# Performance work log

Measured on AMD Instinct MI355X. Metric: run time of the kernel, lower is better.

## Reference

```python
import jax, jax.numpy as jnp
import numpy as np
from jax.scipy.stats import norm

B, IN, H0, H1, OUT = 1024, 2048, 4096, 4096, 1000
EPS_CDF = 1e-5
DECAY = 0.01
NEG_SLOPE = 0.01  # LeakyReLU default slope


def setup_inputs() -> dict:
    key = jax.random.key(0)
    ks = iter(jax.random.split(key, 40))
    rn = lambda shp, s=1.0: s * jax.random.normal(next(ks), shp, dtype=jnp.float32)
    inp = {}
    inp['x'] = rn((B, IN))
    inp['z_w'] = rn((IN,), 0.02)
    for nm, (o, i) in zip(['0', '1', 'o'], [(H0, IN), (H1, H0), (OUT, H1)]):
        inp['w_mu' + nm] = rn((o, i), 0.02)
        inp['w_ls' + nm] = rn((o, i), 0.1) - 2.0  # log-sigma ~ -2 => sigma ~ 0.13
        inp['b_mu' + nm] = rn((o,), 0.02)
        inp['b_ls' + nm] = rn((o,), 0.1) - 2.0
        inp['eps_w' + nm] = rn((o, i))
        inp['eps_b' + nm] = rn((o,))
    inp['pfz0'] = jax.random.uniform(next(ks), (B, H0), dtype=jnp.float32)
    inp['pfz1'] = jax.random.uniform(next(ks), (B, H1), dtype=jnp.float32)
    inp['y'] = jax.random.randint(next(ks), (B,), 0, OUT, dtype=jnp.int32)
    inp['mz0'] = jax.random.randint(next(ks), (B, H0), 0, 2, dtype=jnp.int32)
    inp['mz1'] = jax.random.randint(next(ks), (B, H1), 0, 2, dtype=jnp.int32)
    inp['mask_mu0'] = jax.random.randint(next(ks), (H0,), 0, 2, dtype=jnp.int32)
    inp['mask_mu1'] = jax.random.randint(next(ks), (H1,), 0, 2, dtype=jnp.int32)
    inp['data_set_size'] = 60000
    return inp


def _bayes_layer(h, w_mu, w_ls, b_mu, b_ls, eps_w, eps_b, mz, mask_mu, pfz):
    sw = jnp.exp(w_ls)
    sb = jnp.exp(b_ls)
    w = w_mu + sw * eps_w          # reparameterized weight sample
    b = b_mu + sb * eps_b
    h = h @ w.T + b                # F.linear
    h = jnp.where(h >= 0, h, NEG_SLOPE * h)  # LeakyReLU
    mzf = mz.astype(h.dtype)
    m = mzf * mask_mu.astype(h.dtype)[None, :]   # [B, h]
    mult = m.shape[1] / (m.sum(1) + 1e-6)        # rescale multiplier per sample
    h = h * m * mult[:, None]
    # GFN forward-flow log-prob of the z-mask
    p = jnp.clip(pfz, 1e-6, 1.0 - 1e-6)
    flow = (mzf * jnp.log(p) + (1.0 - mzf) * jnp.log(1.0 - p)).sum()
    # Gaussian CDF likelihood of sampled weights/biases (finite-difference density)
    pw = norm.cdf(w + EPS_CDF, w_mu, sw) - norm.cdf(w - EPS_CDF, w_mu, sw)
    pb = norm.cdf(b + EPS_CDF, b_mu, sb) - norm.cdf(b - EPS_CDF, b_mu, sb)
    flow = flow + jnp.log(pw).sum() + jnp.log(pb).sum()
    return h, flow


def reference(x, z_w, w_mu0, w_ls0, b_mu0, b_ls0, eps_w0, eps_b0,
              w_mu1, w_ls1, b_mu1, b_ls1, eps_w1, eps_b1,
              w_muo, w_lso, b_muo, b_lso, eps_wo, eps_bo,
              pfz0, pfz1, y, mz0, mz1, mask_mu0, mask_mu1, data_set_size):
    loss = (x @ z_w).sum()  # total flow estimator Z
    h, f0 = _bayes_layer(x, w_mu0, w_ls0, b_mu0, b_ls0, eps_w0, eps_b0, mz0, mask_mu0, pfz0)
    loss = loss + f0
    h, f1 = _bayes_layer(h, w_mu1, w_ls1, b_mu1, b_ls1, eps_w1, eps_b1, mz1, mask_mu1, pfz1)
    loss = loss + f1
    # output BayesLinear (sampled)
    wo = w_muo + jnp.exp(w_lso) * eps_wo
    bo = b_muo + jnp.exp(b_lso) * eps_bo
    pred = h @ wo.T + bo  # [B, OUT]
    logp = jax.nn.log_softmax(pred, axis=-1)
    ce = -jnp.take_along_axis(logp, y[:, None].astype(jnp.int32), axis=1).mean()
    loss = loss + jnp.float32(data_set_size) * ce  # NLL
    wd = DECAY * ((w_mu0 ** 2).sum() + jnp.exp(w_ls0).sum()
                  + (w_mu1 ** 2).sum() + jnp.exp(w_ls1).sum())
    loss = (loss + wd) ** 2
    return pred, loss
```

## Files before the change

kernel.cpp:

```cpp
#include <hip/hip_runtime.h>
#include <math.h>

#define B_SZ 1024
#define IN_SZ 2048
#define H0_SZ 4096
#define H1_SZ 4096
#define OUT_SZ 1000

typedef _Float16 f16;
typedef __attribute__((ext_vector_type(4))) _Float16 f16x4;
typedef __attribute__((ext_vector_type(8))) _Float16 f16x8;
typedef __attribute__((ext_vector_type(4))) float f32x4;

#define OFF_N0     0ULL
#define OFF_N1     4ULL
#define OFF_MSUM0  256ULL
#define OFF_MSUM1  4352ULL
#define OFF_CPOS0  8448ULL
#define OFF_CPOS1  24832ULL
#define OFF_IDX0   41216ULL
#define OFF_IDX1   57600ULL
#define OFF_PXZ    73984ULL
#define OFF_PFL    82176ULL
#define OFF_PCE    98560ULL
#define OFF_PB     106752ULL
#define OFF_PW     107776ULL
#define OFF_BS0    370688ULL
#define OFF_BS1    387072ULL
#define OFF_BSO    403456ULL
#define OFF_XH     407552ULL
#define OFF_XL     4601856ULL
#define OFF_H0H    8796160ULL
#define OFF_H0L    17184768ULL
#define OFF_H1H    25573376ULL
#define OFF_H1L    33961984ULL
#define OFF_W0CH   42350592ULL
#define OFF_W0CL   59127808ULL
#define OFF_W1CH   75905024ULL
#define OFF_W1CL   109459456ULL
#define OFF_WOCH   143013888ULL
#define OFF_WOCL   151402496ULL
#define OFF_PART   159791104ULL

#define PSTRIDE_H  2560
#define PSTRIDE_O  1024

__device__ __forceinline__ void gload_lds16(const void* g, void* l)
{
    __builtin_amdgcn_global_load_lds((const __attribute__((address_space(1))) void*)g,
                                     (__attribute__((address_space(3))) void*)l, 16, 0, 0);
}

__device__ __forceinline__ void reduce4_store(double v0, double v1, double v2, double v3,
                                              double* dst)
{
    __shared__ double sh[4][4];
    double v[4] = {v0, v1, v2, v3};
    int lane = threadIdx.x & 63, wid = threadIdx.x >> 6;
#pragma unroll
    for (int a = 0; a < 4; ++a) {
        double x = v[a];
#pragma unroll
        for (int o = 32; o > 0; o >>= 1) x += __shfl_down(x, o, 64);
        if (lane == 0) sh[a][wid] = x;
    }
    __syncthreads();
    if (threadIdx.x == 0) {
        dst[0] = sh[0][0] + sh[0][1] + sh[0][2] + sh[0][3];
        dst[1] = sh[1][0] + sh[1][1] + sh[1][2] + sh[1][3];
        dst[2] = sh[2][0] + sh[2][1] + sh[2][2] + sh[2][3];
        dst[3] = sh[3][0] + sh[3][1] + sh[3][2] + sh[3][3];
    }
}

__device__ __forceinline__ void reduce1_store(double v, double* dst)
{
    __shared__ double sh1[4];
    int lane = threadIdx.x & 63, wid = threadIdx.x >> 6;
#pragma unroll
    for (int o = 32; o > 0; o >>= 1) v += __shfl_down(v, o, 64);
    if (lane == 0) sh1[wid] = v;
    __syncthreads();
    if (threadIdx.x == 0) dst[0] = sh1[0] + sh1[1] + sh1[2] + sh1[3];
}

__global__ __launch_bounds__(1024) void idxbuild_kernel(
    const int* __restrict__ mask0, const int* __restrict__ mask1,
    int* __restrict__ cpos0, int* __restrict__ idx0, int* __restrict__ n0,
    int* __restrict__ cpos1, int* __restrict__ idx1, int* __restrict__ n1)
{
    __shared__ int sh[1024];
    const int t = threadIdx.x;
    for (int pass = 0; pass < 2; ++pass) {
        const int* mask = pass ? mask1 : mask0;
        int* cpos = pass ? cpos1 : cpos0;
        int* idx = pass ? idx1 : idx0;
        int* np = pass ? n1 : n0;
        int4 m = ((const int4*)mask)[t];
        int s = m.x + m.y + m.z + m.w;
        sh[t] = s;
        __syncthreads();
        for (int o = 1; o < 1024; o <<= 1) {
            int v = (t >= o) ? sh[t - o] : 0;
            __syncthreads();
            sh[t] += v;
            __syncthreads();
        }
        int run = sh[t] - s;
        int4 cp;
        cp.x = run; cp.y = run + m.x; cp.z = cp.y + m.y; cp.w = cp.z + m.z;
        ((int4*)cpos)[t] = cp;
        if (m.x) idx[cp.x] = 4 * t + 0;
        if (m.y) idx[cp.y] = 4 * t + 1;
        if (m.z) idx[cp.z] = 4 * t + 2;
        if (m.w) idx[cp.w] = 4 * t + 3;
        if (t == 1023) *np = sh[1023];
        __syncthreads();
    }
}

__global__ __launch_bounds__(256) void splitx_kernel(const float4* __restrict__ x,
                                                     const float4* __restrict__ zw,
                                                     f16x4* __restrict__ xh, f16x4* __restrict__ xl,
                                                     double* __restrict__ pxz)
{
    const int n4 = B_SZ * IN_SZ / 4;
    double s = 0;
    int i = blockIdx.x * blockDim.x + threadIdx.x;
    int stride = gridDim.x * blockDim.x;
    for (; i < n4; i += stride) {
        float4 v = x[i];
        float4 z = zw[i & (IN_SZ / 4 - 1)];
        s += (double)v.x * z.x + (double)v.y * z.y + (double)v.z * z.z + (double)v.w * z.w;
        f16 h0 = (f16)v.x, h1 = (f16)v.y, h2 = (f16)v.z, h3 = (f16)v.w;
        f16x4 hv = {h0, h1, h2, h3};
        f16x4 lv = {(f16)(v.x - (float)h0), (f16)(v.y - (float)h1),
                    (f16)(v.z - (float)h2), (f16)(v.w - (float)h3)};
        xh[i] = hv; xl[i] = lv;
    }
    reduce1_store(s, pxz + blockIdx.x);
}

__global__ __launch_bounds__(256) void flowmsum_kernel(const int* __restrict__ mz,
                                                       const float* __restrict__ pfz,
                                                       const int* __restrict__ maskmu,
                                                       float* __restrict__ msum,
                                                       double* __restrict__ pfl)
{
    const int b = blockIdx.x;
    const int4* m4 = (const int4*)(mz + (size_t)b * 4096);
    const float4* p4 = (const float4*)(pfz + (size_t)b * 4096);
    const int4* k4 = (const int4*)maskmu;
    int s = 0;
    double fl = 0;
    for (int i = threadIdx.x; i < 1024; i += 256) {
        int4 m = m4[i];
        float4 p = p4[i];
        int4 k = k4[i];
        s += m.x * k.x + m.y * k.y + m.z * k.z + m.w * k.w;
        float a0 = fminf(fmaxf(p.x, 1e-6f), 1.0f - 1e-6f);
        float a1 = fminf(fmaxf(p.y, 1e-6f), 1.0f - 1e-6f);
        float a2 = fminf(fmaxf(p.z, 1e-6f), 1.0f - 1e-6f);
        float a3 = fminf(fmaxf(p.w, 1e-6f), 1.0f - 1e-6f);
        fl += (double)logf(m.x ? a0 : 1.0f - a0);
        fl += (double)logf(m.y ? a1 : 1.0f - a1);
        fl += (double)logf(m.z ? a2 : 1.0f - a2);
        fl += (double)logf(m.w ? a3 : 1.0f - a3);
    }
#pragma unroll
    for (int o = 32; o > 0; o >>= 1) {
        s += __shfl_down(s, o, 64);
        fl += __shfl_down(fl, o, 64);
    }
    __shared__ int shi[4];
    __shared__ double shd[4];
    if ((threadIdx.x & 63) == 0) { shi[threadIdx.x >> 6] = s; shd[threadIdx.x >> 6] = fl; }
    __syncthreads();
    if (threadIdx.x == 0) {
        msum[b] = (float)(shi[0] + shi[1] + shi[2] + shi[3]);
        pfl[b] = shd[0] + shd[1] + shd[2] + shd[3];
    }
}

template <int RED>
__global__ __launch_bounds__(256) void bsample_kernel(const float* __restrict__ bmu,
                                                      const float* __restrict__ bls,
                                                      const float* __restrict__ beps,
                                                      float* __restrict__ out, int n,
                                                      double* __restrict__ pb)
{
    int i = blockIdx.x * 256 + threadIdx.x;
    float l = 0.f, e = 0.f;
    if (i < n) {
        l = bls[i]; e = beps[i];
        out[i] = fmaf(__expf(l), e, bmu[i]);
    }
    if (RED) {
        double sls = (i < n) ? (double)l : 0.0;
        double se2 = (i < n) ? (double)e * e : 0.0;
        reduce4_store(sls, se2, 0.0, 0.0, pb + (size_t)blockIdx.x * 4);
    }
}

__global__ __launch_bounds__(256) void wsample_rowc_kernel(
    const float* __restrict__ mu, const float* __restrict__ ls, const float* __restrict__ eps,
    const int* __restrict__ maskR, const int* __restrict__ cposR,
    f16* __restrict__ hi, double* __restrict__ pw)
{
    const int r = blockIdx.x;
    const size_t rb = (size_t)r * IN_SZ;
    const float4* m4 = (const float4*)(mu + rb);
    const float4* l4 = (const float4*)(ls + rb);
    const float4* e4 = (const float4*)(eps + rb);
    const bool wr_ = maskR[r] != 0;
    const int drow = cposR[r];
    f16* hrow = hi + (size_t)drow * IN_SZ;
    double sls = 0, se2 = 0, smu2 = 0, sex = 0;
    for (int i = threadIdx.x; i < IN_SZ / 4; i += 256) {
        float4 m = m4[i], l = l4[i], e = e4[i];
        float g0 = __expf(l.x), g1 = __expf(l.y), g2 = __expf(l.z), g3 = __expf(l.w);
        float w0 = fmaf(g0, e.x, m.x), w1 = fmaf(g1, e.y, m.y);
        float w2 = fmaf(g2, e.z, m.z), w3 = fmaf(g3, e.w, m.w);
        sls += (double)l.x + l.y + l.z + l.w;
        se2 += (double)e.x * e.x + (double)e.y * e.y + (double)e.z * e.z + (double)e.w * e.w;
        smu2 += (double)m.x * m.x + (double)m.y * m.y + (double)m.z * m.z + (double)m.w * m.w;
        sex += (double)g0 + g1 + g2 + g3;
        if (wr_) {
            f16x4 hv = {(f16)w0, (f16)w1, (f16)w2, (f16)w3};
            *(f16x4*)(hrow + i * 4) = hv;
        }
    }
    reduce4_store(sls, se2, smu2, sex, pw + (size_t)r * 4);
}

template <int ROWC, int RED>
__global__ __launch_bounds__(256) void wsample_colc_kernel(
    const float* __restrict__ mu, const float* __restrict__ ls, const float* __restrict__ eps,
    const int* __restrict__ maskR, const int* __restrict__ cposR,
    const int* __restrict__ maskC, const int* __restrict__ cposC, const int* __restrict__ pNc,
    f16* __restrict__ hi, double* __restrict__ pw)
{
    __shared__ __align__(16) f16 ldsH[4096];
    const int r = blockIdx.x;
    const size_t rb = (size_t)r * 4096;
    const float4* m4 = (const float4*)(mu + rb);
    const float4* l4 = (const float4*)(ls + rb);
    const float4* e4 = (const float4*)(eps + rb);
    const bool wr_ = ROWC ? (maskR[r] != 0) : true;
    const int drow = ROWC ? cposR[r] : r;
    const int t = threadIdx.x;
    const f16x8 z8 = {0, 0, 0, 0, 0, 0, 0, 0};
    for (int i = t; i < 512; i += 256) ((f16x8*)ldsH)[i] = z8;
    __syncthreads();
    double sls = 0, se2 = 0, smu2 = 0, sex = 0;
    for (int i = t; i < 1024; i += 256) {
        float4 m = m4[i], l = l4[i], e = e4[i];
        float g0 = __expf(l.x), g1 = __expf(l.y), g2 = __expf(l.z), g3 = __expf(l.w);
        float w0 = fmaf(g0, e.x, m.x), w1 = fmaf(g1, e.y, m.y);
        float w2 = fmaf(g2, e.z, m.z), w3 = fmaf(g3, e.w, m.w);
        if (RED) {
            sls += (double)l.x + l.y + l.z + l.w;
            se2 += (double)e.x * e.x + (double)e.y * e.y + (double)e.z * e.z + (double)e.w * e.w;
            smu2 += (double)m.x * m.x + (double)m.y * m.y + (double)m.z * m.z + (double)m.w * m.w;
            sex += (double)g0 + g1 + g2 + g3;
        }
        if (wr_) {
            int4 mc = ((const int4*)maskC)[i];
            int4 cp = ((const int4*)cposC)[i];
            if (mc.x) ldsH[cp.x] = (f16)w0;
            if (mc.y) ldsH[cp.y] = (f16)w1;
            if (mc.z) ldsH[cp.z] = (f16)w2;
            if (mc.w) ldsH[cp.w] = (f16)w3;
        }
    }
    __syncthreads();
    if (wr_) {
        const int n8 = ((*pNc + 127) >> 7) << 4;
        f16x8* hd = (f16x8*)(hi + (size_t)drow * 4096);
        for (int i = t; i < n8; i += 256) hd[i] = ((const f16x8*)ldsH)[i];
    }
    if (RED) reduce4_store(sls, se2, smu2, sex, pw + (size_t)r * 4);
}

template <int NSPLIT>
__global__ __launch_bounds__(256, 3) void mg128b(
    const f16* __restrict__ Ah, const f16* __restrict__ Al, int SA,
    const f16* __restrict__ Wh, int SW,
    const int* __restrict__ pN, int NFIX,
    const int* __restrict__ pK, int KFIX,
    float* __restrict__ P0, float* __restrict__ P1,
    float* __restrict__ P2, float* __restrict__ P3,
    float* __restrict__ P4, float* __restrict__ P5,
    float* __restrict__ P6, float* __restrict__ P7, int pstride)
{
    const int bid = blockIdx.x;
    const int c8 = bid & 7, j = bid >> 3;
    int nt, mt, z;
    if (NSPLIT == 4) {
        const int p = c8 + 8 * (j % 10);
        nt = p >> 2; z = p & 3; mt = j / 10;
    } else {
        const int p = c8 + 8 * (j & 7);
        nt = p >> 3; z = p & 7; mt = j >> 3;
    }
    const int nvalid = pN ? *pN : NFIX;
    const int bn = nt * 128;
    if (bn >= nvalid) return;
    const int bm = mt * 128;
    const int kvalid = pK ? *pK : KFIX;
    const int ktiles = (kvalid + 31) >> 5;
    const int prt = (ktiles + NSPLIT - 1) / NSPLIT;
    const int kt0 = z * prt;
    const int kt1 = min(ktiles, kt0 + prt);
    float* Cf = (z == 0) ? P0 : (z == 1) ? P1 : (z == 2) ? P2 : (z == 3) ? P3
              : (z == 4) ? P4 : (z == 5) ? P5 : (z == 6) ? P6 : P7;

    __shared__ __align__(16) f16 lds[2][12288];
    const int tid = threadIdx.x;
    const int wv = tid >> 6, lane = tid & 63;
    const int wr = wv >> 1, wc = wv & 1;
    const int l15 = lane & 15, l4 = lane >> 4;

    const f16* sg[6];
    int ldst[6];
#pragma unroll
    for (int i = 0; i < 6; ++i) {
        const int c = wv * 6 + i;
        const int plane = c >> 3, cidx = c & 7;
        const f16* base = (plane == 0) ? Ah : (plane == 1) ? Al : Wh;
        const int S_ = (plane < 2) ? SA : SW;
        const int rowb = (plane < 2) ? bm : bn;
        sg[i] = base + (size_t)(rowb + cidx * 16 + l15) * S_ + l4 * 8;
        ldst[i] = c * 512 + lane * 8;
    }

#define STAGE(KT, B) do { \
        _Pragma("unroll") \
        for (int i_ = 0; i_ < 6; ++i_) \
            gload_lds16(sg[i_] + (size_t)(KT) * 32, &lds[B][ldst[i_]]); \
    } while (0)

    f32x4 acc[4][4];
#pragma unroll
    for (int m = 0; m < 4; ++m)
#pragma unroll
        for (int n = 0; n < 4; ++n) acc[m][n] = (f32x4){0.f, 0.f, 0.f, 0.f};

    if (kt0 < kt1) {
        STAGE(kt0, 0);
        int cur = 0;
        for (int kt = kt0; kt < kt1; ++kt) {
            asm volatile("s_waitcnt vmcnt(0)" ::: "memory");
            __builtin_amdgcn_s_barrier();
            __builtin_amdgcn_sched_barrier(0);
            if (kt + 1 < kt1) STAGE(kt + 1, cur ^ 1);
            __builtin_amdgcn_sched_barrier(0);
            const f16* L = &lds[cur][0];
            f16x8 ah[4], al[4], wh[4];
#pragma unroll
            for (int m = 0; m < 4; ++m) {
                ah[m] = *(const f16x8*)(L + (wr * 4 + m) * 512 + lane * 8);
                al[m] = *(const f16x8*)(L + 4096 + (wr * 4 + m) * 512 + lane * 8);
            }
#pragma unroll
            for (int n = 0; n < 4; ++n)
                wh[n] = *(const f16x8*)(L + 8192 + (wc * 4 + n) * 512 + lane * 8);
#pragma unroll
            for (int m = 0; m < 4; ++m)
#pragma unroll
                for (int n = 0; n < 4; ++n)
                    acc[m][n] = __builtin_amdgcn_mfma_f32_16x16x32_f16(ah[m], wh[n], acc[m][n], 0, 0, 0);
#pragma unroll
            for (int m = 0; m < 4; ++m)
#pragma unroll
                for (int n = 0; n < 4; ++n)
                    acc[m][n] = __builtin_amdgcn_mfma_f32_16x16x32_f16(al[m], wh[n], acc[m][n], 0, 0, 0);
            cur ^= 1;
        }
    }
#undef STAGE

#pragma unroll
    for (int n = 0; n < 4; ++n) {
        const int c = bn + wc * 64 + n * 16 + l15;
        if (c >= pstride) continue;
#pragma unroll
        for (int m = 0; m < 4; ++m)
#pragma unroll
            for (int j2 = 0; j2 < 4; ++j2) {
                const int row = bm + wr * 64 + m * 16 + l4 * 4 + j2;
                Cf[(size_t)row * pstride + c] = acc[m][n][j2];
            }
    }
}

__global__ __launch_bounds__(256) void combine4_kernel(
    const float* __restrict__ PA, const float* __restrict__ PB,
    const float* __restrict__ PC, const float* __restrict__ PD, int pstride,
    const float* __restrict__ bsamp, const int* __restrict__ idx,
    const int* __restrict__ mz, const float* __restrict__ msum,
    const int* __restrict__ pN,
    f16* __restrict__ Chh, f16* __restrict__ Chl)
{
    const int nv = *pN;
    const int bn = blockIdx.x * 64;
    const int bm = blockIdx.y * 64;
    const int t = threadIdx.x;
    const int c0 = bn + (t & 15) * 4;
    const int r0 = bm + (t >> 4);
#pragma unroll
    for (int rr = 0; rr < 4; ++rr) {
        const int row = r0 + rr * 16;
        const float mult = 4096.0f / (msum[row] + 1e-6f);
        float sv[4] = {0.f, 0.f, 0.f, 0.f};
        if (c0 < pstride) {
            float4 a = *(const float4*)(PA + (size_t)row * pstride + c0);
            float4 b = *(const float4*)(PB + (size_t)row * pstride + c0);
            float4 c = *(const float4*)(PC + (size_t)row * pstride + c0);
            float4 d = *(const float4*)(PD + (size_t)row * pstride + c0);
            sv[0] = (a.x + b.x) + (c.x + d.x);
            sv[1] = (a.y + b.y) + (c.y + d.y);
            sv[2] = (a.z + b.z) + (c.z + d.z);
            sv[3] = (a.w + b.w) + (c.w + d.w);
        }
        f16 hh[4], ll[4];
#pragma unroll
        for (int jj = 0; jj < 4; ++jj) {
            const int c = c0 + jj;
            float v = 0.f;
            if (c < nv) {
                const int orig = idx[c];
                v = sv[jj] + bsamp[orig];
                v = v >= 0.f ? v : 0.01f * v;
                v = v * (float)mz[(size_t)row * 4096 + orig] * mult;
            }
            hh[jj] = (f16)v;
            ll[jj] = (f16)(v - (float)hh[jj]);
        }
        f16x4 hv = {hh[0], hh[1], hh[2], hh[3]};
        f16x4 lv = {ll[0], ll[1], ll[2], ll[3]};
        *(f16x4*)(Chh + (size_t)row * 4096 + c0) = hv;
        *(f16x4*)(Chl + (size_t)row * 4096 + c0) = lv;
    }
}

__global__ __launch_bounds__(256) void ce_fused8_kernel(
    const float* __restrict__ Q0, const float* __restrict__ Q1,
    const float* __restrict__ Q2, const float* __restrict__ Q3,
    const float* __restrict__ Q4, const float* __restrict__ Q5,
    const float* __restrict__ Q6, const float* __restrict__ Q7,
    const float* __restrict__ bso, const int* __restrict__ y,
    float* __restrict__ pred, double* __restrict__ pce)
{
    const int b = blockIdx.x;
    float mx = -1e30f;
    for (int jj = threadIdx.x; jj < OUT_SZ; jj += 256) {
        const size_t o = (size_t)b * PSTRIDE_O + jj;
        float v = ((Q0[o] + Q1[o]) + (Q2[o] + Q3[o]))
                + ((Q4[o] + Q5[o]) + (Q6[o] + Q7[o])) + bso[jj];
        pred[(size_t)b * OUT_SZ + jj] = v;
        mx = fmaxf(mx, v);
    }
#pragma unroll
    for (int o = 32; o > 0; o >>= 1) mx = fmaxf(mx, __shfl_down(mx, o, 64));
    __shared__ float sm[4];
    if ((threadIdx.x & 63) == 0) sm[threadIdx.x >> 6] = mx;
    __syncthreads();
    mx = fmaxf(fmaxf(sm[0], sm[1]), fmaxf(sm[2], sm[3]));
    double se = 0;
    for (int jj = threadIdx.x; jj < OUT_SZ; jj += 256)
        se += (double)__expf(pred[(size_t)b * OUT_SZ + jj] - mx);
#pragma unroll
    for (int o = 32; o > 0; o >>= 1) se += __shfl_down(se, o, 64);
    __shared__ double sd[4];
    if ((threadIdx.x & 63) == 0) sd[threadIdx.x >> 6] = se;
    __syncthreads();
    if (threadIdx.x == 0) {
        double lse = (double)mx + log(sd[0] + sd[1] + sd[2] + sd[3]);
        pce[b] = lse - (double)pred[(size_t)b * OUT_SZ + y[b]];
    }
}

__global__ __launch_bounds__(256) void finalize_kernel(
    const double* __restrict__ PXZ, const double* __restrict__ PFL,
    const double* __restrict__ PCE, const double* __restrict__ PB,
    const double* __restrict__ PW, const int* __restrict__ dss, float* __restrict__ out)
{
    const int t = threadIdx.x;
    double xz = 0, fl = 0, ce = 0, ls = 0, e2 = 0, mu2 = 0, ex = 0;
    for (int i = t; i < 1024; i += 256) xz += PXZ[i];
    for (int i = t; i < 2048; i += 256) fl += PFL[i];
    for (int i = t; i < 1024; i += 256) ce += PCE[i];
    for (int i = t; i < 8192; i += 256) {
        const double* p = PW + (size_t)i * 4;
        ls += p[0]; e2 += p[1]; mu2 += p[2]; ex += p[3];
    }
    if (t < 32) { ls += PB[t * 4]; e2 += PB[t * 4 + 1]; }
    __shared__ double sh[7][4];
    double v[7] = {xz, fl, ce, ls, e2, mu2, ex};
    const int lane = t & 63, wid = t >> 6;
#pragma unroll
    for (int a = 0; a < 7; ++a) {
        double x = v[a];
#pragma unroll
        for (int o = 32; o > 0; o >>= 1) x += __shfl_down(x, o, 64);
        if (lane == 0) sh[a][wid] = x;
    }
    __syncthreads();
    if (t == 0) {
        double T[7];
#pragma unroll
        for (int a = 0; a < 7; ++a) T[a] = sh[a][0] + sh[a][1] + sh[a][2] + sh[a][3];
        const double NTOT = 25174016.0;
        double cst = NTOT * (log(2.0e-5) - 0.91893853320467274178);
        double loss = T[0]
                    + cst - T[3] - 0.5 * T[4]
                    + T[1]
                    + (double)(*dss) * (T[2] / (double)B_SZ)
                    + 0.01 * (T[5] + T[6]);
        out[(size_t)B_SZ * OUT_SZ] = (float)(loss * loss);
    }
}

extern "C" void kernel_launch(void* const* d_in, const int* in_sizes, int n_in,
                              void* d_out, int out_size, void* d_ws, size_t ws_size,
                              hipStream_t stream)
{
    const float* x = (const float*)d_in[0];
    const float* zw = (const float*)d_in[1];
    const float* wmu0 = (const float*)d_in[2];
    const float* wls0 = (const float*)d_in[3];
    const float* bmu0 = (const float*)d_in[4];
    const float* bls0 = (const float*)d_in[5];
    const float* weps0 = (const float*)d_in[6];
    const float* beps0 = (const float*)d_in[7];
    const float* wmu1 = (const float*)d_in[8];
    const float* wls1 = (const float*)d_in[9];
    const float* bmu1 = (const float*)d_in[10];
    const float* bls1 = (const float*)d_in[11];
    const float* weps1 = (const float*)d_in[12];
    const float* beps1 = (const float*)d_in[13];
    const float* wmuo = (const float*)d_in[14];
    const float* wlso = (const float*)d_in[15];
    const float* bmuo = (const float*)d_in[16];
    const float* blso = (const float*)d_in[17];
    const float* wepso = (const float*)d_in[18];
    const float* bepso = (const float*)d_in[19];
    const float* pfz0 = (const float*)d_in[20];
    const float* pfz1 = (const float*)d_in[21];
    const int* y = (const int*)d_in[22];
    const int* mz0 = (const int*)d_in[23];
    const int* mz1 = (const int*)d_in[24];
    const int* mmu0 = (const int*)d_in[25];
    const int* mmu1 = (const int*)d_in[26];
    const int* dss = (const int*)d_in[27];

    char* ws = (char*)d_ws;
    int* n0p = (int*)(ws + OFF_N0);
    int* n1p = (int*)(ws + OFF_N1);
    float* msum0 = (float*)(ws + OFF_MSUM0);
    float* msum1 = (float*)(ws + OFF_MSUM1);
    int* cpos0 = (int*)(ws + OFF_CPOS0);
    int* cpos1 = (int*)(ws + OFF_CPOS1);
    int* idx0 = (int*)(ws + OFF_IDX0);
    int* idx1 = (int*)(ws + OFF_IDX1);
    double* PXZ = (double*)(ws + OFF_PXZ);
    double* PFL = (double*)(ws + OFF_PFL);
    double* PCE = (double*)(ws + OFF_PCE);
    double* PB = (double*)(ws + OFF_PB);
    double* PW = (double*)(ws + OFF_PW);
    float* bs0 = (float*)(ws + OFF_BS0);
    float* bs1 = (float*)(ws + OFF_BS1);
    float* bso = (float*)(ws + OFF_BSO);
    f16* xh = (f16*)(ws + OFF_XH);
    f16* xl = (f16*)(ws + OFF_XL);
    f16* h0h = (f16*)(ws + OFF_H0H);
    f16* h0l = (f16*)(ws + OFF_H0L);
    f16* h1h = (f16*)(ws + OFF_H1H);
    f16* h1l = (f16*)(ws + OFF_H1L);
    f16* w0ch = (f16*)(ws + OFF_W0CH);
    f16* w1ch = (f16*)(ws + OFF_W1CH);
    f16* woch = (f16*)(ws + OFF_WOCH);
    float* out = (float*)d_out;

    float* A0 = (float*)(ws + OFF_H1H);
    float* A1 = (float*)(ws + OFF_PART);
    float* A2 = (float*)(ws + OFF_W0CL);
    float* A3 = (float*)(ws + OFF_W1CL);
    float* B0 = (float*)(ws + OFF_W0CH);
    float* B1 = (float*)(ws + OFF_W0CL);
    float* B2 = (float*)(ws + OFF_W1CL);
    float* B3 = (float*)(ws + OFF_PART);
    float* Q[8];
    for (int i = 0; i < 8; ++i) Q[i] = (float*)(ws + OFF_W0CH + (size_t)i * 4194304ULL);

    splitx_kernel<<<1024, 256, 0, stream>>>((const float4*)x, (const float4*)zw,
                                            (f16x4*)xh, (f16x4*)xl, PXZ);
    flowmsum_kernel<<<B_SZ, 256, 0, stream>>>(mz0, pfz0, mmu0, msum0, PFL);
    flowmsum_kernel<<<B_SZ, 256, 0, stream>>>(mz1, pfz1, mmu1, msum1, PFL + 1024);
    bsample_kernel<1><<<16, 256, 0, stream>>>(bmu0, bls0, beps0, bs0, H0_SZ, PB);
    bsample_kernel<1><<<16, 256, 0, stream>>>(bmu1, bls1, beps1, bs1, H1_SZ, PB + 16 * 4);
    bsample_kernel<0><<<4, 256, 0, stream>>>(bmuo, blso, bepso, bso, OUT_SZ, nullptr);
    idxbuild_kernel<<<1, 1024, 0, stream>>>(mmu0, mmu1, cpos0, idx0, n0p, cpos1, idx1, n1p);

    wsample_rowc_kernel<<<H0_SZ, 256, 0, stream>>>(wmu0, wls0, weps0, mmu0, cpos0, w0ch, PW);
    wsample_colc_kernel<1, 1><<<H1_SZ, 256, 0, stream>>>(wmu1, wls1, weps1, mmu1, cpos1,
                                                         mmu0, cpos0, n0p, w1ch,
                                                         PW + (size_t)4096 * 4);
    wsample_colc_kernel<0, 0><<<OUT_SZ, 256, 0, stream>>>(wmuo, wlso, wepso, nullptr, nullptr,
                                                          mmu1, cpos1, n1p, woch, nullptr);

    mg128b<4><<<640, 256, 0, stream>>>(
        xh, xl, IN_SZ, w0ch, IN_SZ, n0p, 0, nullptr, IN_SZ,
        A0, A1, A2, A3, nullptr, nullptr, nullptr, nullptr, PSTRIDE_H);
    combine4_kernel<<<dim3(64, 16), 256, 0, stream>>>(
        A0, A1, A2, A3, PSTRIDE_H, bs0, idx0, mz0, msum0, n0p, h0h, h0l);
    mg128b<4><<<640, 256, 0, stream>>>(
        h0h, h0l, 4096, w1ch, 4096, n1p, 0, n0p, 0,
        B0, B1, B2, B3, nullptr, nullptr, nullptr, nullptr, PSTRIDE_H);
    combine4_kernel<<<dim3(64, 16), 256, 0, stream>>>(
        B0, B1, B2, B3, PSTRIDE_H, bs1, idx1, mz1, msum1, n1p, h1h, h1l);
    mg128b<8><<<512, 256, 0, stream>>>(
        h1h, h1l, 4096, woch, 4096, nullptr, OUT_SZ, n1p, 0,
        Q[0], Q[1], Q[2], Q[3], Q[4], Q[5], Q[6], Q[7], PSTRIDE_O);

    ce_fused8_kernel<<<B_SZ, 256, 0, stream>>>(Q[0], Q[1], Q[2], Q[3], Q[4], Q[5], Q[6], Q[7],
                                               bso, y, out, PCE);
    finalize_kernel<<<1, 256, 0, stream>>>(PXZ, PFL, PCE, PB, PW, dss, out);
}
```

Baseline: 306.6 us.

## Fuse all prep kernels into one role-dispatched launch and parallelize idxbuild

Merges the splitx, flow/msum, bias-sample and three weight-sample kernels into a single prep_kernel that picks a role from blockIdx, so there are fewer launches and the small stages fill the GPU together. idxbuild now runs its two masks in two blocks instead of two serial passes. It also switches the per-element double accumulations to float partial sums, which lowers double-precision work but slightly changes rounding. splitx now uses 256 blocks instead of 1024, and the finalize reduction reads only 256 partials to match.

```diff
diff --git a/kernel.cpp b/kernel.cpp
--- a/kernel.cpp
+++ b/kernel.cpp
@@ -45,6 +45,16 @@
 #define PSTRIDE_H  2560
 #define PSTRIDE_O  1024
 
+#define RB_W1   4096
+#define RB_WO   5096
+#define RB_W0   9192
+#define RB_FL0  10216
+#define RB_FL1  11240
+#define RB_SX   11496
+#define RB_B0   11512
+#define RB_B1   11528
+#define RB_BO   11532
+
 __device__ __forceinline__ void gload_lds16(const void* g, void* l)
 {
     __builtin_amdgcn_global_load_lds((const __attribute__((address_space(1))) void*)g,
@@ -91,63 +101,56 @@
 {
     __shared__ int sh[1024];
     const int t = threadIdx.x;
-    for (int pass = 0; pass < 2; ++pass) {
-        const int* mask = pass ? mask1 : mask0;
-        int* cpos = pass ? cpos1 : cpos0;
-        int* idx = pass ? idx1 : idx0;
-        int* np = pass ? n1 : n0;
-        int4 m = ((const int4*)mask)[t];
-        int s = m.x + m.y + m.z + m.w;
-        sh[t] = s;
+    const int pass = blockIdx.x;
+    const int* mask = pass ? mask1 : mask0;
+    int* cpos = pass ? cpos1 : cpos0;
+    int* idx = pass ? idx1 : idx0;
+    int* np = pass ? n1 : n0;
+    int4 m = ((const int4*)mask)[t];
+    int s = m.x + m.y + m.z + m.w;
+    sh[t] = s;
+    __syncthreads();
+    for (int o = 1; o < 1024; o <<= 1) {
+        int v = (t >= o) ? sh[t - o] : 0;
         __syncthreads();
-        for (int o = 1; o < 1024; o <<= 1) {
-            int v = (t >= o) ? sh[t - o] : 0;
-            __syncthreads();
-            sh[t] += v;
-            __syncthreads();
-        }
-        int run = sh[t] - s;
-        int4 cp;
-        cp.x = run; cp.y = run + m.x; cp.z = cp.y + m.y; cp.w = cp.z + m.z;
-        ((int4*)cpos)[t] = cp;
-        if (m.x) idx[cp.x] = 4 * t + 0;
-        if (m.y) idx[cp.y] = 4 * t + 1;
-        if (m.z) idx[cp.z] = 4 * t + 2;
-        if (m.w) idx[cp.w] = 4 * t + 3;
-        if (t == 1023) *np = sh[1023];
+        sh[t] += v;
         __syncthreads();
     }
-}
-
-__global__ __launch_bounds__(256) void splitx_kernel(const float4* __restrict__ x,
-                                                     const float4* __restrict__ zw,
-                                                     f16x4* __restrict__ xh, f16x4* __restrict__ xl,
-                                                     double* __restrict__ pxz)
+    int run = sh[t] - s;
+    int4 cp;
+    cp.x = run; cp.y = run + m.x; cp.z = cp.y + m.y; cp.w = cp.z + m.z;
+    ((int4*)cpos)[t] = cp;
+    if (m.x) idx[cp.x] = 4 * t + 0;
+    if (m.y) idx[cp.y] = 4 * t + 1;
+    if (m.z) idx[cp.z] = 4 * t + 2;
+    if (m.w) idx[cp.w] = 4 * t + 3;
+    if (t == 1023) *np = sh[1023];
+}
+
+
+__device__ void role_splitx(int rb, const float4* x, const float4* zw,
+                            f16x4* xh, f16x4* xl, double* pxz)
 {
     const int n4 = B_SZ * IN_SZ / 4;
     double s = 0;
-    int i = blockIdx.x * blockDim.x + threadIdx.x;
-    int stride = gridDim.x * blockDim.x;
+    int i = rb * 256 + threadIdx.x;
+    const int stride = 256 * 256;
     for (; i < n4; i += stride) {
         float4 v = x[i];
         float4 z = zw[i & (IN_SZ / 4 - 1)];
-        s += (double)v.x * z.x + (double)v.y * z.y + (double)v.z * z.z + (double)v.w * z.w;
+        s += (double)((v.x * z.x + v.y * z.y) + (v.z * z.z + v.w * z.w));
         f16 h0 = (f16)v.x, h1 = (f16)v.y, h2 = (f16)v.z, h3 = (f16)v.w;
         f16x4 hv = {h0, h1, h2, h3};
         f16x4 lv = {(f16)(v.x - (float)h0), (f16)(v.y - (float)h1),
                     (f16)(v.z - (float)h2), (f16)(v.w - (float)h3)};
         xh[i] = hv; xl[i] = lv;
     }
-    reduce1_store(s, pxz + blockIdx.x);
-}
-
-__global__ __launch_bounds__(256) void flowmsum_kernel(const int* __restrict__ mz,
-                                                       const float* __restrict__ pfz,
-                                                       const int* __restrict__ maskmu,
-                                                       float* __restrict__ msum,
-                                                       double* __restrict__ pfl)
-{
-    const int b = blockIdx.x;
+    reduce1_store(s, pxz + rb);
+}
+
+__device__ void role_flow(int b, const int* mz, const float* pfz, const int* maskmu,
+                          float* msum, double* pfl)
+{
     const int4* m4 = (const int4*)(mz + (size_t)b * 4096);
     const float4* p4 = (const float4*)(pfz + (size_t)b * 4096);
     const int4* k4 = (const int4*)maskmu;
@@ -162,10 +165,11 @@
         float a1 = fminf(fmaxf(p.y, 1e-6f), 1.0f - 1e-6f);
         float a2 = fminf(fmaxf(p.z, 1e-6f), 1.0f - 1e-6f);
         float a3 = fminf(fmaxf(p.w, 1e-6f), 1.0f - 1e-6f);
-        fl += (double)logf(m.x ? a0 : 1.0f - a0);
-        fl += (double)logf(m.y ? a1 : 1.0f - a1);
-        fl += (double)logf(m.z ? a2 : 1.0f - a2);
-        fl += (double)logf(m.w ? a3 : 1.0f - a3);
+        float g0 = logf(m.x ? a0 : 1.0f - a0);
+        float g1 = logf(m.y ? a1 : 1.0f - a1);
+        float g2 = logf(m.z ? a2 : 1.0f - a2);
+        float g3 = logf(m.w ? a3 : 1.0f - a3);
+        fl += (double)((g0 + g1) + (g2 + g3));
     }
 #pragma unroll
     for (int o = 32; o > 0; o >>= 1) {
@@ -183,13 +187,10 @@
 }
 
 template <int RED>
-__global__ __launch_bounds__(256) void bsample_kernel(const float* __restrict__ bmu,
-                                                      const float* __restrict__ bls,
-                                                      const float* __restrict__ beps,
-                                                      float* __restrict__ out, int n,
-                                                      double* __restrict__ pb)
-{
-    int i = blockIdx.x * 256 + threadIdx.x;
+__device__ void role_bsample(int rb, const float* bmu, const float* bls, const float* beps,
+                             float* out, int n, double* pb)
+{
+    int i = rb * 256 + threadIdx.x;
     float l = 0.f, e = 0.f;
     if (i < n) {
         l = bls[i]; e = beps[i];
@@ -198,20 +199,17 @@
     if (RED) {
         double sls = (i < n) ? (double)l : 0.0;
         double se2 = (i < n) ? (double)e * e : 0.0;
-        reduce4_store(sls, se2, 0.0, 0.0, pb + (size_t)blockIdx.x * 4);
-    }
-}
-
-__global__ __launch_bounds__(256) void wsample_rowc_kernel(
-    const float* __restrict__ mu, const float* __restrict__ ls, const float* __restrict__ eps,
-    const int* __restrict__ maskR, const int* __restrict__ cposR,
-    f16* __restrict__ hi, double* __restrict__ pw)
-{
-    const int r = blockIdx.x;
-    const size_t rb = (size_t)r * IN_SZ;
-    const float4* m4 = (const float4*)(mu + rb);
-    const float4* l4 = (const float4*)(ls + rb);
-    const float4* e4 = (const float4*)(eps + rb);
+        reduce4_store(sls, se2, 0.0, 0.0, pb + (size_t)rb * 4);
+    }
+}
+
+__device__ void role_w0(int r, const float* mu, const float* ls, const float* eps,
+                        const int* maskR, const int* cposR, f16* hi, double* pw)
+{
+    const size_t rbb = (size_t)r * IN_SZ;
+    const float4* m4 = (const float4*)(mu + rbb);
+    const float4* l4 = (const float4*)(ls + rbb);
+    const float4* e4 = (const float4*)(eps + rbb);
     const bool wr_ = maskR[r] != 0;
     const int drow = cposR[r];
     f16* hrow = hi + (size_t)drow * IN_SZ;
@@ -221,10 +219,10 @@
         float g0 = __expf(l.x), g1 = __expf(l.y), g2 = __expf(l.z), g3 = __expf(l.w);
         float w0 = fmaf(g0, e.x, m.x), w1 = fmaf(g1, e.y, m.y);
         float w2 = fmaf(g2, e.z, m.z), w3 = fmaf(g3, e.w, m.w);
-        sls += (double)l.x + l.y + l.z + l.w;
-        se2 += (double)e.x * e.x + (double)e.y * e.y + (double)e.z * e.z + (double)e.w * e.w;
-        smu2 += (double)m.x * m.x + (double)m.y * m.y + (double)m.z * m.z + (double)m.w * m.w;
-        sex += (double)g0 + g1 + g2 + g3;
+        sls += (double)((l.x + l.y) + (l.z + l.w));
+        se2 += (double)((e.x * e.x + e.y * e.y) + (e.z * e.z + e.w * e.w));
+        smu2 += (double)((m.x * m.x + m.y * m.y) + (m.z * m.z + m.w * m.w));
+        sex += (double)((g0 + g1) + (g2 + g3));
         if (wr_) {
             f16x4 hv = {(f16)w0, (f16)w1, (f16)w2, (f16)w3};
             *(f16x4*)(hrow + i * 4) = hv;
@@ -233,24 +231,23 @@
     reduce4_store(sls, se2, smu2, sex, pw + (size_t)r * 4);
 }
 
+__shared__ __align__(16) f16 g_ldsH[4096];
+
 template <int ROWC, int RED>
-__global__ __launch_bounds__(256) void wsample_colc_kernel(
-    const float* __restrict__ mu, const float* __restrict__ ls, const float* __restrict__ eps,
-    const int* __restrict__ maskR, const int* __restrict__ cposR,
-    const int* __restrict__ maskC, const int* __restrict__ cposC, const int* __restrict__ pNc,
-    f16* __restrict__ hi, double* __restrict__ pw)
-{
-    __shared__ __align__(16) f16 ldsH[4096];
-    const int r = blockIdx.x;
-    const size_t rb = (size_t)r * 4096;
-    const float4* m4 = (const float4*)(mu + rb);
-    const float4* l4 = (const float4*)(ls + rb);
-    const float4* e4 = (const float4*)(eps + rb);
+__device__ void role_colc(int r, const float* mu, const float* ls, const float* eps,
+                          const int* maskR, const int* cposR,
+                          const int* maskC, const int* cposC, const int* pNc,
+                          f16* hi, double* pw)
+{
+    const size_t rbb = (size_t)r * 4096;
+    const float4* m4 = (const float4*)(mu + rbb);
+    const float4* l4 = (const float4*)(ls + rbb);
+    const float4* e4 = (const float4*)(eps + rbb);
     const bool wr_ = ROWC ? (maskR[r] != 0) : true;
     const int drow = ROWC ? cposR[r] : r;
     const int t = threadIdx.x;
     const f16x8 z8 = {0, 0, 0, 0, 0, 0, 0, 0};
-    for (int i = t; i < 512; i += 256) ((f16x8*)ldsH)[i] = z8;
+    for (int i = t; i < 512; i += 256) ((f16x8*)g_ldsH)[i] = z8;
     __syncthreads();
     double sls = 0, se2 = 0, smu2 = 0, sex = 0;
     for (int i = t; i < 1024; i += 256) {
@@ -259,27 +256,72 @@
         float w0 = fmaf(g0, e.x, m.x), w1 = fmaf(g1, e.y, m.y);
         float w2 = fmaf(g2, e.z, m.z), w3 = fmaf(g3, e.w, m.w);
         if (RED) {
-            sls += (double)l.x + l.y + l.z + l.w;
-            se2 += (double)e.x * e.x + (double)e.y * e.y + (double)e.z * e.z + (double)e.w * e.w;
-            smu2 += (double)m.x * m.x + (double)m.y * m.y + (double)m.z * m.z + (double)m.w * m.w;
-            sex += (double)g0 + g1 + g2 + g3;
+            sls += (double)((l.x + l.y) + (l.z + l.w));
+            se2 += (double)((e.x * e.x + e.y * e.y) + (e.z * e.z + e.w * e.w));
+            smu2 += (double)((m.x * m.x + m.y * m.y) + (m.z * m.z + m.w * m.w));
+            sex += (double)((g0 + g1) + (g2 + g3));
         }
         if (wr_) {
             int4 mc = ((const int4*)maskC)[i];
             int4 cp = ((const int4*)cposC)[i];
-            if (mc.x) ldsH[cp.x] = (f16)w0;
-            if (mc.y) ldsH[cp.y] = (f16)w1;
-            if (mc.z) ldsH[cp.z] = (f16)w2;
-            if (mc.w) ldsH[cp.w] = (f16)w3;
+            if (mc.x) g_ldsH[cp.x] = (f16)w0;
+            if (mc.y) g_ldsH[cp.y] = (f16)w1;
+            if (mc.z) g_ldsH[cp.z] = (f16)w2;
+            if (mc.w) g_ldsH[cp.w] = (f16)w3;
         }
     }
     __syncthreads();
     if (wr_) {
         const int n8 = ((*pNc + 127) >> 7) << 4;
         f16x8* hd = (f16x8*)(hi + (size_t)drow * 4096);
-        for (int i = t; i < n8; i += 256) hd[i] = ((const f16x8*)ldsH)[i];
+        for (int i = t; i < n8; i += 256) hd[i] = ((const f16x8*)g_ldsH)[i];
     }
     if (RED) reduce4_store(sls, se2, smu2, sex, pw + (size_t)r * 4);
+}
+
+__global__ __launch_bounds__(256) void prep_kernel(
+    const float* __restrict__ x, const float* __restrict__ zw,
+    const float* __restrict__ wmu0, const float* __restrict__ wls0, const float* __restrict__ weps0,
+    const float* __restrict__ bmu0, const float* __restrict__ bls0, const float* __restrict__ beps0,
+    const float* __restrict__ wmu1, const float* __restrict__ wls1, const float* __restrict__ weps1,
+    const float* __restrict__ bmu1, const float* __restrict__ bls1, const float* __restrict__ beps1,
+    const float* __restrict__ wmuo, const float* __restrict__ wlso, const float* __restrict__ wepso,
+    const float* __restrict__ bmuo, const float* __restrict__ blso, const float* __restrict__ bepso,
+    const float* __restrict__ pfz0, const float* __restrict__ pfz1,
+    const int* __restrict__ mz0, const int* __restrict__ mz1,
+    const int* __restrict__ mmu0, const int* __restrict__ mmu1,
+    const int* __restrict__ cpos0, const int* __restrict__ cpos1,
+    const int* __restrict__ n0p, const int* __restrict__ n1p,
+    f16* __restrict__ xh, f16* __restrict__ xl,
+    f16* __restrict__ w0ch, f16* __restrict__ w1ch, f16* __restrict__ woch,
+    float* __restrict__ bs0, float* __restrict__ bs1, float* __restrict__ bso,
+    float* __restrict__ msum0, float* __restrict__ msum1,
+    double* __restrict__ PXZ, double* __restrict__ PFL,
+    double* __restrict__ PB, double* __restrict__ PW)
+{
+    const int b = blockIdx.x;
+    if (b < RB_W1) {
+        role_colc<1, 1>(b, wmu1, wls1, weps1, mmu1, cpos1, mmu0, cpos0, n0p,
+                        w1ch, PW + (size_t)4096 * 4);
+    } else if (b < RB_WO) {
+        role_colc<0, 0>(b - RB_W1, wmuo, wlso, wepso, nullptr, nullptr, mmu1, cpos1, n1p,
+                        woch, nullptr);
+    } else if (b < RB_W0) {
+        role_w0(b - RB_WO, wmu0, wls0, weps0, mmu0, cpos0, w0ch, PW);
+    } else if (b < RB_FL0) {
+        role_flow(b - RB_W0, mz0, pfz0, mmu0, msum0, PFL);
+    } else if (b < RB_FL1) {
+        role_flow(b - RB_FL0, mz1, pfz1, mmu1, msum1, PFL + 1024);
+    } else if (b < RB_SX) {
+        role_splitx(b - RB_FL1, (const float4*)x, (const float4*)zw,
+                    (f16x4*)xh, (f16x4*)xl, PXZ);
+    } else if (b < RB_B0) {
+        role_bsample<1>(b - RB_SX, bmu0, bls0, beps0, bs0, H0_SZ, PB);
+    } else if (b < RB_B1) {
+        role_bsample<1>(b - RB_B0, bmu1, bls1, beps1, bs1, H1_SZ, PB + 16 * 4);
+    } else {
+        role_bsample<0>(b - RB_B1, bmuo, blso, bepso, bso, OUT_SZ, nullptr);
+    }
 }
 
 template <int NSPLIT>
@@ -488,7 +530,7 @@
 {
     const int t = threadIdx.x;
     double xz = 0, fl = 0, ce = 0, ls = 0, e2 = 0, mu2 = 0, ex = 0;
-    for (int i = t; i < 1024; i += 256) xz += PXZ[i];
+    if (t < 256) { if (t < 256) xz += PXZ[t]; }
     for (int i = t; i < 2048; i += 256) fl += PFL[i];
     for (int i = t; i < 1024; i += 256) ce += PCE[i];
     for (int i = t; i < 8192; i += 256) {
@@ -594,21 +636,15 @@
     float* Q[8];
     for (int i = 0; i < 8; ++i) Q[i] = (float*)(ws + OFF_W0CH + (size_t)i * 4194304ULL);
 
-    splitx_kernel<<<1024, 256, 0, stream>>>((const float4*)x, (const float4*)zw,
-                                            (f16x4*)xh, (f16x4*)xl, PXZ);
-    flowmsum_kernel<<<B_SZ, 256, 0, stream>>>(mz0, pfz0, mmu0, msum0, PFL);
-    flowmsum_kernel<<<B_SZ, 256, 0, stream>>>(mz1, pfz1, mmu1, msum1, PFL + 1024);
-    bsample_kernel<1><<<16, 256, 0, stream>>>(bmu0, bls0, beps0, bs0, H0_SZ, PB);
-    bsample_kernel<1><<<16, 256, 0, stream>>>(bmu1, bls1, beps1, bs1, H1_SZ, PB + 16 * 4);
-    bsample_kernel<0><<<4, 256, 0, stream>>>(bmuo, blso, bepso, bso, OUT_SZ, nullptr);
-    idxbuild_kernel<<<1, 1024, 0, stream>>>(mmu0, mmu1, cpos0, idx0, n0p, cpos1, idx1, n1p);
-
-    wsample_rowc_kernel<<<H0_SZ, 256, 0, stream>>>(wmu0, wls0, weps0, mmu0, cpos0, w0ch, PW);
-    wsample_colc_kernel<1, 1><<<H1_SZ, 256, 0, stream>>>(wmu1, wls1, weps1, mmu1, cpos1,
-                                                         mmu0, cpos0, n0p, w1ch,
-                                                         PW + (size_t)4096 * 4);
-    wsample_colc_kernel<0, 0><<<OUT_SZ, 256, 0, stream>>>(wmuo, wlso, wepso, nullptr, nullptr,
-                                                          mmu1, cpos1, n1p, woch, nullptr);
+    idxbuild_kernel<<<2, 1024, 0, stream>>>(mmu0, mmu1, cpos0, idx0, n0p, cpos1, idx1, n1p);
+
+    prep_kernel<<<RB_BO, 256, 0, stream>>>(
+        x, zw, wmu0, wls0, weps0, bmu0, bls0, beps0,
+        wmu1, wls1, weps1, bmu1, bls1, beps1,
+        wmuo, wlso, wepso, bmuo, blso, bepso,
+        pfz0, pfz1, mz0, mz1, mmu0, mmu1, cpos0, cpos1, n0p, n1p,
+        xh, xl, w0ch, w1ch, woch, bs0, bs1, bso, msum0, msum1,
+        PXZ, PFL, PB, PW);
 
     mg128b<4><<<640, 256, 0, stream>>>(
         xh, xl, IN_SZ, w0ch, IN_SZ, n0p, 0, nullptr, IN_SZ,
```

After: 271.7 us. 1.13x faster.
